# Kernel optimization log

Hardware: AMD Instinct MI355X
Metric: run time of the kernel (lower is better)

Reference implementation:

```python
import jax, jax.numpy as jnp
import numpy as np
import math

B, N, CS, CZ, CH, H, PQK, PV = 1, 1024, 384, 128, 16, 12, 4, 8
INF, EPS = 1e5, 1e-8


def quat_to_rot(q):
    w, x, y, z = q[..., 0], q[..., 1], q[..., 2], q[..., 3]
    r = jnp.stack([
        1 - 2 * (y * y + z * z), 2 * (x * y - w * z), 2 * (x * z + w * y),
        2 * (x * y + w * z), 1 - 2 * (x * x + z * z), 2 * (y * z - w * x),
        2 * (x * z - w * y), 2 * (y * z + w * x), 1 - 2 * (x * x + y * y),
    ], axis=-1)
    return r.reshape(q.shape[:-1] + (3, 3))


def setup_inputs() -> dict:
    key = jax.random.key(0)
    ks = jax.random.split(key, 12)
    sc = 0.02
    s = jax.random.normal(ks[0], (B, N, CS), jnp.float32)
    z = jax.random.normal(ks[1], (B, N, N, CZ), jnp.float32)
    quat = jax.random.normal(ks[2], (B, N, 4), jnp.float32)
    rot = quat_to_rot(quat / jnp.linalg.norm(quat, axis=-1, keepdims=True))
    trans = jax.random.normal(ks[3], (B, N, 3), jnp.float32)
    mask = jnp.ones((B, N), jnp.float32)
    wq = jax.random.normal(ks[4], (CS, H * CH), jnp.float32) * sc
    bq = jnp.zeros((H * CH,), jnp.float32)
    wkv = jax.random.normal(ks[5], (CS, 2 * H * CH), jnp.float32) * sc
    bkv = jnp.zeros((2 * H * CH,), jnp.float32)
    wqp = jax.random.normal(ks[6], (CS, H * PQK * 3), jnp.float32) * sc
    bqp = jnp.zeros((H * PQK * 3,), jnp.float32)
    wkvp = jax.random.normal(ks[7], (CS, H * (PQK + PV) * 3), jnp.float32) * sc
    bkvp = jnp.zeros((H * (PQK + PV) * 3,), jnp.float32)
    wb = jax.random.normal(ks[8], (CZ, H), jnp.float32) * sc
    bb = jnp.zeros((H,), jnp.float32)
    head_w = jax.random.normal(ks[9], (H,), jnp.float32) * 0.1 + 0.5413  # softplus^-1(1)
    dcat = H * (CZ + CH + PV * 4)
    wout = jax.random.normal(ks[10], (dcat, CS), jnp.float32) * sc
    bout = jnp.zeros((CS,), jnp.float32)
    return dict(s=s, z=z, rot=rot, trans=trans, mask=mask, wq=wq, bq=bq,
                wkv=wkv, bkv=bkv, wqp=wqp, bqp=bqp, wkvp=wkvp, bkvp=bkvp,
                wb=wb, bb=bb, head_w=head_w, wout=wout, bout=bout)


def reference(s, z, rot, trans, mask, wq, bq, wkv, bkv, wqp, bqp, wkvp, bkvp,
              wb, bb, head_w, wout, bout):
    # scalar q/k/v: [B,N,H,CH]
    q = (s @ wq + bq).reshape(B, N, H, CH)
    kv = (s @ wkv + bkv).reshape(B, N, H, 2 * CH)
    k, v = kv[..., :CH], kv[..., CH:]

    def make_pts(raw, P):
        # raw layout: [x-coords | y-coords | z-coords], each of width H*P
        pts = jnp.swapaxes(raw.reshape(B, N, 3, H * P), -1, -2)  # [B,N,H*P,3]
        pts = jnp.einsum('bnxy,bnpy->bnpx', rot, pts) + trans[:, :, None, :]
        return pts.reshape(B, N, H, P, 3)

    q_pts = make_pts(s @ wqp + bqp, PQK)                 # [B,N,H,PQK,3] global frame
    kv_pts = make_pts(s @ wkvp + bkvp, PQK + PV)
    k_pts, v_pts = kv_pts[..., :PQK, :], kv_pts[..., PQK:, :]

    # scalar attention + pair bias: [B,H,N,N]
    a = jnp.einsum('bihc,bjhc->bhij', q, k) * math.sqrt(1.0 / (3 * CH))
    bias = z @ wb + bb                                    # [B,N,N,H]
    a = a + math.sqrt(1.0 / 3) * jnp.transpose(bias, (0, 3, 1, 2))

    # point attention via ||q-k||^2 = |q|^2 + |k|^2 - 2 q.k (summed over pts & xyz)
    hw = jax.nn.softplus(head_w) * math.sqrt(1.0 / (3 * (PQK * 9.0 / 2)))  # [H]
    qn = jnp.sum(q_pts ** 2, axis=(-1, -2))               # [B,N,H]
    kn = jnp.sum(k_pts ** 2, axis=(-1, -2))
    cross = jnp.einsum('bihpx,bjhpx->bhij', q_pts, k_pts)
    sqd = (jnp.transpose(qn, (0, 2, 1))[..., None]
           + jnp.transpose(kn, (0, 2, 1))[:, :, None, :]
           - 2.0 * cross)                                 # [B,H,N,N]
    a = a - 0.5 * hw[None, :, None, None] * sqd

    sqm = INF * (mask[:, :, None] * mask[:, None, :] - 1.0)  # [B,N,N]
    a = jax.nn.softmax(a + sqm[:, None], axis=-1)

    # outputs
    o = jnp.einsum('bhij,bjhc->bihc', a, v).reshape(B, N, H * CH)
    o_pt = jnp.einsum('bhij,bjhpx->bihpx', a, v_pts)      # [B,N,H,PV,3] global
    o_pt = jnp.einsum('bnyx,bnhpy->bnhpx', rot, o_pt - trans[:, :, None, None, :])  # invert_apply
    o_pt_norm = jnp.sqrt(jnp.sum(o_pt ** 2, axis=-1) + EPS).reshape(B, N, H * PV)
    o_pt3 = o_pt.reshape(B, N, H * PV, 3)
    o_pair = jnp.einsum('bhij,bijc->bihc', a, z).reshape(B, N, H * CZ)

    cat = jnp.concatenate(
        [o, o_pt3[..., 0], o_pt3[..., 1], o_pt3[..., 2], o_pt_norm, o_pair], axis=-1)
    return cat @ wout + bout
```

## Files before the change

kernel.cpp:

```cpp
#include <hip/hip_runtime.h>
#include <hip/hip_bf16.h>
#include <math.h>

#define NN   1024
#define CS   384
#define CZ   128
#define HH   12
#define HCH  192
#define QPR  144
#define DCAT 2112
#define PROJW 1152
#define INF_ 100000.0f

#define SC_QK 0.14433756729740643f
#define SC_B  0.5773502691896258f
#define SC_PT 0.13608276348795434f

__device__ __forceinline__ float dot4(float4 a, float4 b) {
  return a.x * b.x + a.y * b.y + a.z * b.z + a.w * b.w;
}
__device__ __forceinline__ float bf2f(unsigned short u) {
  unsigned int v = ((unsigned int)u) << 16;
  float f; __builtin_memcpy(&f, &v, 4); return f;
}
__device__ __forceinline__ unsigned short f2bf(float f) {
  __hip_bfloat16 h = __float2bfloat16(f);
  unsigned short u; __builtin_memcpy(&u, &h, 2); return u;
}

__global__ void prep(const float* __restrict__ wb, const float* __restrict__ head_w,
                     float* __restrict__ wb_t, float* __restrict__ hw)
{
  int t = threadIdx.x;
  for (int idx = t; idx < CZ * HH; idx += 256) {
    int c = idx % HH == idx % HH ? idx / HH : 0;
    int h = idx - c * HH;
    wb_t[h * CZ + c] = wb[idx];
  }
  if (t < HH) {
    float x = head_w[t];
    float sp = (x > 20.f) ? x : log1pf(__expf(x));
    hw[t] = sp * SC_PT;
  }
}

__global__ __launch_bounds__(256) void proj_all(
    const float* __restrict__ s,
    const float* __restrict__ wq, const float* __restrict__ bq,
    const float* __restrict__ wkv, const float* __restrict__ bkv,
    const float* __restrict__ wqp, const float* __restrict__ bqp,
    const float* __restrict__ wkvp, const float* __restrict__ bkvp,
    float* __restrict__ proj)
{
  __shared__ float s_lds[8 * CS];
  const int n0 = blockIdx.x * 8;
  for (int idx = threadIdx.x; idx < 8 * CS; idx += 256)
    s_lds[idx] = s[(size_t)(n0 + idx / CS) * CS + (idx % CS)];
  __syncthreads();

  const int gc = blockIdx.y * 128 + (threadIdx.x & 31) * 4;
  const int rg = threadIdx.x >> 5;
  const float* wp; const float* bp; int OUT, lc;
  if (gc < 192)      { wp = wq;   bp = bq;   OUT = 192; lc = gc; }
  else if (gc < 576) { wp = wkv;  bp = bkv;  OUT = 384; lc = gc - 192; }
  else if (gc < 720) { wp = wqp;  bp = bqp;  OUT = 144; lc = gc - 576; }
  else               { wp = wkvp; bp = bkvp; OUT = 432; lc = gc - 720; }

  float a0 = 0.f, a1 = 0.f, a2 = 0.f, a3 = 0.f;
  const float* srow = &s_lds[rg * CS];
#pragma unroll 4
  for (int kk = 0; kk < CS; kk++) {
    float sv = srow[kk];
    float4 w4 = *reinterpret_cast<const float4*>(&wp[(size_t)kk * OUT + lc]);
    a0 += sv * w4.x; a1 += sv * w4.y; a2 += sv * w4.z; a3 += sv * w4.w;
  }
  float* o = proj + (size_t)(n0 + rg) * PROJW + gc;
  o[0] = a0 + bp[lc]; o[1] = a1 + bp[lc + 1];
  o[2] = a2 + bp[lc + 2]; o[3] = a3 + bp[lc + 3];
}

__global__ __launch_bounds__(256) void ipa_transform(
    const float* __restrict__ proj, const float* __restrict__ rot,
    const float* __restrict__ trans,
    float* __restrict__ kc, float* __restrict__ vc,
    float* __restrict__ q_pts, float* __restrict__ kpc,
    float* __restrict__ vpc, float* __restrict__ qn, float* __restrict__ knc)
{
  const int n = blockIdx.x, tid = threadIdx.x;
  const float* pr = proj + (size_t)n * PROJW;
  __shared__ float R[9], T[3], sq_q[48], sq_k[48];
  if (tid < 9) R[tid] = rot[n * 9 + tid];
  if (tid < 3) T[tid] = trans[n * 3 + tid];
  __syncthreads();
  if (tid < HCH) {
    int h = tid >> 4, c = tid & 15;
    kc[(size_t)(h * 16 + c) * NN + n] = pr[192 + h * 32 + c];
    vc[(size_t)(h * 16 + c) * NN + n] = pr[192 + h * 32 + 16 + c];
  }
  if (tid < 48) {
    float r0 = pr[576 + tid], r1 = pr[576 + 48 + tid], r2 = pr[576 + 96 + tid];
    float x = R[0] * r0 + R[1] * r1 + R[2] * r2 + T[0];
    float y = R[3] * r0 + R[4] * r1 + R[5] * r2 + T[1];
    float z = R[6] * r0 + R[7] * r1 + R[8] * r2 + T[2];
    q_pts[(size_t)n * QPR + tid * 3 + 0] = x;
    q_pts[(size_t)n * QPR + tid * 3 + 1] = y;
    q_pts[(size_t)n * QPR + tid * 3 + 2] = z;
    sq_q[tid] = x * x + y * y + z * z;
  }
  if (tid >= 64 && tid < 208) {
    int t = tid - 64;
    float r0 = pr[720 + t], r1 = pr[720 + 144 + t], r2 = pr[720 + 288 + t];
    float x = R[0] * r0 + R[1] * r1 + R[2] * r2 + T[0];
    float y = R[3] * r0 + R[4] * r1 + R[5] * r2 + T[1];
    float z = R[6] * r0 + R[7] * r1 + R[8] * r2 + T[2];
    int h = t / 12, pp = t % 12;
    if (pp < 4) {
      int d = pp * 3;
      kpc[(size_t)(h * 12 + d + 0) * NN + n] = x;
      kpc[(size_t)(h * 12 + d + 1) * NN + n] = y;
      kpc[(size_t)(h * 12 + d + 2) * NN + n] = z;
      sq_k[h * 4 + pp] = x * x + y * y + z * z;
    } else {
      int d = (pp - 4) * 3;
      vpc[(size_t)(h * 24 + d + 0) * NN + n] = x;
      vpc[(size_t)(h * 24 + d + 1) * NN + n] = y;
      vpc[(size_t)(h * 24 + d + 2) * NN + n] = z;
    }
  }
  __syncthreads();
  if (tid < HH) {
    float a = 0.f, b = 0.f;
#pragma unroll
    for (int p = 0; p < 4; p++) { a += sq_q[tid * 4 + p]; b += sq_k[tid * 4 + p]; }
    qn[n * HH + tid] = a;
    knc[(size_t)tid * NN + n] = b;
  }
}

__global__ __launch_bounds__(256) void bias_pass(
    const float* __restrict__ z, const float* __restrict__ wb_t,
    __hip_bfloat16* __restrict__ B)
{
  __shared__ float wb_s[HH * CZ];
  __shared__ float bias_s[HH * 128];
  const int i = blockIdx.y;
  const int jb = blockIdx.x * 128;
  const int tid = threadIdx.x;
  const int jl = tid >> 2, csub = tid & 3;

  for (int e = tid; e < HH * CZ; e += 256) wb_s[e] = wb_t[e];
  __syncthreads();

  const float* zb = z + ((size_t)i * NN + jb + jl) * CZ + csub * 4;
  float4 zq0[8], zq1[8];
#pragma unroll
  for (int k8 = 0; k8 < 8; k8++)
    zq0[k8] = *reinterpret_cast<const float4*>(&zb[k8 * 16]);
#pragma unroll
  for (int k8 = 0; k8 < 8; k8++)
    zq1[k8] = *reinterpret_cast<const float4*>(&zb[(size_t)64 * CZ + k8 * 16]);

  float bd0[HH], bd1[HH];
#pragma unroll
  for (int h = 0; h < HH; h++) { bd0[h] = 0.f; bd1[h] = 0.f; }

#pragma unroll
  for (int k8 = 0; k8 < 8; k8++) {
    const int c = csub * 4 + k8 * 16;
#pragma unroll
    for (int h = 0; h < HH; h++) {
      float4 wv = *reinterpret_cast<const float4*>(&wb_s[h * CZ + c]);
      bd0[h] += dot4(zq0[k8], wv);
      bd1[h] += dot4(zq1[k8], wv);
    }
  }
#pragma unroll
  for (int h = 0; h < HH; h++) {
    bd0[h] += __shfl_xor(bd0[h], 1); bd0[h] += __shfl_xor(bd0[h], 2);
    bd1[h] += __shfl_xor(bd1[h], 1); bd1[h] += __shfl_xor(bd1[h], 2);
  }
  if (csub == 0) {
#pragma unroll
    for (int h = 0; h < HH; h++) {
      bias_s[h * 128 + jl] = bd0[h];
      bias_s[h * 128 + 64 + jl] = bd1[h];
    }
  }
  __syncthreads();
  for (int e = tid; e < HH * 128; e += 256) {
    int h = e >> 7, j2 = e & 127;
    B[((size_t)i * HH + h) * NN + jb + j2] = __float2bfloat16(bias_s[e]);
  }
}

__global__ __launch_bounds__(256) void ipa_attn(
    const float* __restrict__ kc, const float* __restrict__ kpc,
    const float* __restrict__ knc, const float* __restrict__ vc,
    const float* __restrict__ vpc, const float* __restrict__ proj,
    const float* __restrict__ q_pts, const float* __restrict__ qn,
    const float* __restrict__ bb, const float* __restrict__ hw,
    const float* __restrict__ mask,
    __hip_bfloat16* __restrict__ A, float* __restrict__ cat,
    float* __restrict__ optb)
{
  const int h = blockIdx.y;
  const int i = blockIdx.x * 4 + (threadIdx.x >> 6);
  const int lane = threadIdx.x & 63;

  const float* qb = proj + (size_t)i * PROJW + h * 16;
  const float4 q0 = *reinterpret_cast<const float4*>(qb);
  const float4 q1 = *reinterpret_cast<const float4*>(qb + 4);
  const float4 q2 = *reinterpret_cast<const float4*>(qb + 8);
  const float4 q3 = *reinterpret_cast<const float4*>(qb + 12);
  const float* pb = q_pts + (size_t)i * QPR + h * 12;
  const float4 p0 = *reinterpret_cast<const float4*>(pb);
  const float4 p1 = *reinterpret_cast<const float4*>(pb + 4);
  const float4 p2 = *reinterpret_cast<const float4*>(pb + 8);
  const float qnv = qn[i * HH + h];
  const float bbv = bb[h];
  const float hwv = hw[h];
  const float mi = mask[i];

  const float* kch  = kc  + (size_t)h * 16 * NN;
  const float* kpch = kpc + (size_t)h * 12 * NN;
  const float* knch = knc + (size_t)h * NN;
  const float* vch  = vc  + (size_t)h * 16 * NN;
  const float* vpch = vpc + (size_t)h * 24 * NN;
  __hip_bfloat16* Arow = A + ((size_t)i * HH + h) * NN;

  float4 av[4];
#pragma unroll
  for (int t = 0; t < 4; t++) {
    const int j = t * 256 + lane * 4;
    float4 d = {0, 0, 0, 0};
#pragma unroll
    for (int c = 0; c < 16; c++) {
      const float qc = (c < 4 ? (&q0.x)[c] : c < 8 ? (&q1.x)[c - 4]
                       : c < 12 ? (&q2.x)[c - 8] : (&q3.x)[c - 12]);
      float4 kv = *reinterpret_cast<const float4*>(&kch[(size_t)c * NN + j]);
      d.x += qc * kv.x; d.y += qc * kv.y; d.z += qc * kv.z; d.w += qc * kv.w;
    }
    float4 cr = {0, 0, 0, 0};
#pragma unroll
    for (int dd = 0; dd < 12; dd++) {
      const float pc = (dd < 4 ? (&p0.x)[dd] : dd < 8 ? (&p1.x)[dd - 4]
                        : (&p2.x)[dd - 8]);
      float4 kv = *reinterpret_cast<const float4*>(&kpch[(size_t)dd * NN + j]);
      cr.x += pc * kv.x; cr.y += pc * kv.y; cr.z += pc * kv.z; cr.w += pc * kv.w;
    }
    float4 kn4 = *reinterpret_cast<const float4*>(&knch[j]);
    ushort4 bu = *reinterpret_cast<const ushort4*>(&Arow[j]);
    float4 m4 = *reinterpret_cast<const float4*>(&mask[j]);
    av[t].x = SC_QK * d.x + SC_B * (bf2f(bu.x) + bbv)
              - 0.5f * hwv * (qnv + kn4.x - 2.f * cr.x) + INF_ * (mi * m4.x - 1.f);
    av[t].y = SC_QK * d.y + SC_B * (bf2f(bu.y) + bbv)
              - 0.5f * hwv * (qnv + kn4.y - 2.f * cr.y) + INF_ * (mi * m4.y - 1.f);
    av[t].z = SC_QK * d.z + SC_B * (bf2f(bu.z) + bbv)
              - 0.5f * hwv * (qnv + kn4.z - 2.f * cr.z) + INF_ * (mi * m4.z - 1.f);
    av[t].w = SC_QK * d.w + SC_B * (bf2f(bu.w) + bbv)
              - 0.5f * hwv * (qnv + kn4.w - 2.f * cr.w) + INF_ * (mi * m4.w - 1.f);
  }

  float m = av[0].x;
#pragma unroll
  for (int t = 0; t < 4; t++) {
    m = fmaxf(m, av[t].x); m = fmaxf(m, av[t].y);
    m = fmaxf(m, av[t].z); m = fmaxf(m, av[t].w);
  }
  for (int off = 32; off; off >>= 1) m = fmaxf(m, __shfl_xor(m, off));
  float ssum = 0.f;
#pragma unroll
  for (int t = 0; t < 4; t++) {
    av[t].x = __expf(av[t].x - m); ssum += av[t].x;
    av[t].y = __expf(av[t].y - m); ssum += av[t].y;
    av[t].z = __expf(av[t].z - m); ssum += av[t].z;
    av[t].w = __expf(av[t].w - m); ssum += av[t].w;
  }
  for (int off = 32; off; off >>= 1) ssum += __shfl_xor(ssum, off);
  const float inv = 1.f / ssum;
#pragma unroll
  for (int t = 0; t < 4; t++) {
    const int j = t * 256 + lane * 4;
    av[t].x *= inv; av[t].y *= inv; av[t].z *= inv; av[t].w *= inv;
    ushort4 st;
    st.x = f2bf(av[t].x); st.y = f2bf(av[t].y);
    st.z = f2bf(av[t].z); st.w = f2bf(av[t].w);
    *reinterpret_cast<ushort4*>(&Arow[j]) = st;
  }

  float oacc[16], wacc[24];
#pragma unroll
  for (int c = 0; c < 16; c++) oacc[c] = 0.f;
#pragma unroll
  for (int d = 0; d < 24; d++) wacc[d] = 0.f;
#pragma unroll
  for (int t = 0; t < 4; t++) {
    const int j = t * 256 + lane * 4;
    const float4 a4 = av[t];
#pragma unroll
    for (int c = 0; c < 16; c++) {
      float4 vv = *reinterpret_cast<const float4*>(&vch[(size_t)c * NN + j]);
      oacc[c] += dot4(a4, vv);
    }
#pragma unroll
    for (int d = 0; d < 24; d++) {
      float4 wv = *reinterpret_cast<const float4*>(&vpch[(size_t)d * NN + j]);
      wacc[d] += dot4(a4, wv);
    }
  }
  for (int off = 32; off; off >>= 1) {
#pragma unroll
    for (int c = 0; c < 16; c++) oacc[c] += __shfl_xor(oacc[c], off);
#pragma unroll
    for (int d = 0; d < 24; d++) wacc[d] += __shfl_xor(wacc[d], off);
  }
  if (lane == 0) {
    float* cr = cat + (size_t)i * DCAT + h * 16;
#pragma unroll
    for (int c = 0; c < 16; c++) cr[c] = oacc[c];
    float* ob = optb + ((size_t)i * HH + h) * 24;
#pragma unroll
    for (int d = 0; d < 24; d++) ob[d] = wacc[d];
  }
}

__global__ __launch_bounds__(256) void opair_pass(
    const float* __restrict__ z, const __hip_bfloat16* __restrict__ A,
    float* __restrict__ partial)
{
  __shared__ float A_ls[256 * HH];
  __shared__ float red[HH * CZ];
  const int sp = blockIdx.x, i = blockIdx.y;
  const int jb = sp * 256;
  const int tid = threadIdx.x;
  const int c4 = (tid & 31) * 4, jsub = tid >> 5;

  for (int e = tid; e < HH * 64; e += 256) {
    int h = e >> 6, j4 = (e & 63) * 4;
    ushort4 au = *reinterpret_cast<const ushort4*>(
        &A[((size_t)i * HH + h) * NN + jb + j4]);
    A_ls[(j4 + 0) * HH + h] = bf2f(au.x);
    A_ls[(j4 + 1) * HH + h] = bf2f(au.y);
    A_ls[(j4 + 2) * HH + h] = bf2f(au.z);
    A_ls[(j4 + 3) * HH + h] = bf2f(au.w);
  }
  for (int e = tid; e < HH * CZ; e += 256) red[e] = 0.f;
  __syncthreads();

  float4 acc[HH];
#pragma unroll
  for (int h = 0; h < HH; h++) acc[h] = make_float4(0.f, 0.f, 0.f, 0.f);

  const float* zrow = z + ((size_t)i * NN + jb + jsub * 32) * CZ + c4;
  const float* arow = &A_ls[jsub * 32 * HH];
  for (int j0 = 0; j0 < 32; j0 += 4) {
#pragma unroll
    for (int jj = 0; jj < 4; jj++) {
      const int j = j0 + jj;
      float4 zq = *reinterpret_cast<const float4*>(&zrow[(size_t)j * CZ]);
      float4 a0 = *reinterpret_cast<const float4*>(&arow[j * HH]);
      float4 a1 = *reinterpret_cast<const float4*>(&arow[j * HH + 4]);
      float4 a2 = *reinterpret_cast<const float4*>(&arow[j * HH + 8]);
      acc[0].x += a0.x * zq.x; acc[0].y += a0.x * zq.y;
      acc[0].z += a0.x * zq.z; acc[0].w += a0.x * zq.w;
      acc[1].x += a0.y * zq.x; acc[1].y += a0.y * zq.y;
      acc[1].z += a0.y * zq.z; acc[1].w += a0.y * zq.w;
      acc[2].x += a0.z * zq.x; acc[2].y += a0.z * zq.y;
      acc[2].z += a0.z * zq.z; acc[2].w += a0.z * zq.w;
      acc[3].x += a0.w * zq.x; acc[3].y += a0.w * zq.y;
      acc[3].z += a0.w * zq.z; acc[3].w += a0.w * zq.w;
      acc[4].x += a1.x * zq.x; acc[4].y += a1.x * zq.y;
      acc[4].z += a1.x * zq.z; acc[4].w += a1.x * zq.w;
      acc[5].x += a1.y * zq.x; acc[5].y += a1.y * zq.y;
      acc[5].z += a1.y * zq.z; acc[5].w += a1.y * zq.w;
      acc[6].x += a1.z * zq.x; acc[6].y += a1.z * zq.y;
      acc[6].z += a1.z * zq.z; acc[6].w += a1.z * zq.w;
      acc[7].x += a1.w * zq.x; acc[7].y += a1.w * zq.y;
      acc[7].z += a1.w * zq.z; acc[7].w += a1.w * zq.w;
      acc[8].x += a2.x * zq.x; acc[8].y += a2.x * zq.y;
      acc[8].z += a2.x * zq.z; acc[8].w += a2.x * zq.w;
      acc[9].x += a2.y * zq.x; acc[9].y += a2.y * zq.y;
      acc[9].z += a2.y * zq.z; acc[9].w += a2.y * zq.w;
      acc[10].x += a2.z * zq.x; acc[10].y += a2.z * zq.y;
      acc[10].z += a2.z * zq.z; acc[10].w += a2.z * zq.w;
      acc[11].x += a2.w * zq.x; acc[11].y += a2.w * zq.y;
      acc[11].z += a2.w * zq.z; acc[11].w += a2.w * zq.w;
    }
  }
  for (int s = 0; s < 8; s++) {
    __syncthreads();
    if (jsub == s) {
#pragma unroll
      for (int h = 0; h < HH; h++) {
        red[h * CZ + c4 + 0] += acc[h].x;
        red[h * CZ + c4 + 1] += acc[h].y;
        red[h * CZ + c4 + 2] += acc[h].z;
        red[h * CZ + c4 + 3] += acc[h].w;
      }
    }
  }
  __syncthreads();
  float* pp = partial + ((size_t)(i * 4 + sp)) * (HH * CZ);
  for (int e = tid; e < HH * CZ; e += 256) pp[e] = red[e];
}

__global__ __launch_bounds__(256) void opair_reduce(
    const float* __restrict__ partial, const float* __restrict__ optb,
    const float* __restrict__ rot, const float* __restrict__ trans,
    float* __restrict__ cat)
{
  const int i = blockIdx.x, tid = threadIdx.x;
  __shared__ float R_s[9], T_s[3];
  if (tid < 9) R_s[tid] = rot[i * 9 + tid];
  if (tid < 3) T_s[tid] = trans[i * 3 + tid];
  __syncthreads();

  const float* pp = partial + ((size_t)i * 4) * (HH * CZ);
  for (int e = tid; e < HH * CZ; e += 256) {
    float v = pp[e] + pp[HH * CZ + e] + pp[2 * HH * CZ + e] + pp[3 * HH * CZ + e];
    cat[(size_t)i * DCAT + 576 + e] = v;
  }
  if (tid < 96) {
    int h = tid >> 3, p = tid & 7;
    const float* ob = optb + ((size_t)i * HH + h) * 24 + p * 3;
    float gx = ob[0] - T_s[0];
    float gy = ob[1] - T_s[1];
    float gz = ob[2] - T_s[2];
    float lx = R_s[0] * gx + R_s[3] * gy + R_s[6] * gz;
    float ly = R_s[1] * gx + R_s[4] * gy + R_s[7] * gz;
    float lz = R_s[2] * gx + R_s[5] * gy + R_s[8] * gz;
    float* catr = cat + (size_t)i * DCAT;
    catr[192 + 0 * 96 + h * 8 + p] = lx;
    catr[192 + 1 * 96 + h * 8 + p] = ly;
    catr[192 + 2 * 96 + h * 8 + p] = lz;
    catr[480 + h * 8 + p] = sqrtf(lx * lx + ly * ly + lz * lz + 1e-8f);
  }
}

__global__ __launch_bounds__(256) void out_gemm(
    const float* __restrict__ cat, const float* __restrict__ wout,
    const float* __restrict__ bout, float* __restrict__ out)
{
  __shared__ float c_lds[4 * DCAT];
  const int n0 = blockIdx.x * 4;
  const int cq = blockIdx.y * 128 + (threadIdx.x & 63) * 2;
  const int rg = threadIdx.x >> 6;
  for (int idx = threadIdx.x; idx < 4 * DCAT; idx += 256) {
    int r = idx / DCAT, kk = idx - r * DCAT;
    c_lds[idx] = cat[(size_t)(n0 + r) * DCAT + kk];
  }
  __syncthreads();
  float a0 = 0.f, a1 = 0.f;
  const float* crow = &c_lds[rg * DCAT];
#pragma unroll 4
  for (int kk = 0; kk < DCAT; kk++) {
    float cv = crow[kk];
    float2 w2 = *reinterpret_cast<const float2*>(&wout[(size_t)kk * CS + cq]);
    a0 += cv * w2.x; a1 += cv * w2.y;
  }
  float* o = out + (size_t)(n0 + rg) * CS + cq;
  o[0] = a0 + bout[cq]; o[1] = a1 + bout[cq + 1];
}

extern "C" void kernel_launch(void* const* d_in, const int* in_sizes, int n_in,
                              void* d_out, int out_size, void* d_ws, size_t ws_size,
                              hipStream_t stream) {
  const float* s      = (const float*)d_in[0];
  const float* z      = (const float*)d_in[1];
  const float* rot    = (const float*)d_in[2];
  const float* trans  = (const float*)d_in[3];
  const float* mask   = (const float*)d_in[4];
  const float* wq     = (const float*)d_in[5];
  const float* bq     = (const float*)d_in[6];
  const float* wkv    = (const float*)d_in[7];
  const float* bkv    = (const float*)d_in[8];
  const float* wqp    = (const float*)d_in[9];
  const float* bqp    = (const float*)d_in[10];
  const float* wkvp   = (const float*)d_in[11];
  const float* bkvp   = (const float*)d_in[12];
  const float* wb     = (const float*)d_in[13];
  const float* bb     = (const float*)d_in[14];
  const float* head_w = (const float*)d_in[15];
  const float* wout   = (const float*)d_in[16];
  const float* bout   = (const float*)d_in[17];
  float* out = (float*)d_out;

  float* ws = (float*)d_ws;
  float* proj_buf = ws;
  float* kc_buf   = proj_buf + (size_t)NN * PROJW;
  float* vc_buf   = kc_buf + (size_t)HH * 16 * NN;
  float* kpc_buf  = vc_buf + (size_t)HH * 16 * NN;
  float* vpc_buf  = kpc_buf + (size_t)HH * 12 * NN;
  float* knc_buf  = vpc_buf + (size_t)HH * 24 * NN;
  float* qpts_buf = knc_buf + (size_t)HH * NN;
  float* qn_buf   = qpts_buf + (size_t)NN * QPR;
  float* wbt_buf  = qn_buf + NN * HH;
  float* hw_buf   = wbt_buf + HH * CZ;
  float* optb_buf = hw_buf + 16;
  float* cat_buf  = optb_buf + (size_t)NN * HH * 24;
  float* part_buf = cat_buf + (size_t)NN * DCAT;
  __hip_bfloat16* A_buf =
      (__hip_bfloat16*)(part_buf + (size_t)4 * NN * HH * CZ);

  prep<<<dim3(1), dim3(256), 0, stream>>>(wb, head_w, wbt_buf, hw_buf);
  proj_all<<<dim3(NN / 8, 9), dim3(256), 0, stream>>>(
      s, wq, bq, wkv, bkv, wqp, bqp, wkvp, bkvp, proj_buf);
  ipa_transform<<<dim3(NN), dim3(256), 0, stream>>>(
      proj_buf, rot, trans, kc_buf, vc_buf, qpts_buf, kpc_buf, vpc_buf,
      qn_buf, knc_buf);
  bias_pass<<<dim3(8, NN), dim3(256), 0, stream>>>(z, wbt_buf, A_buf);
  ipa_attn<<<dim3(NN / 4, HH), dim3(256), 0, stream>>>(
      kc_buf, kpc_buf, knc_buf, vc_buf, vpc_buf, proj_buf, qpts_buf,
      qn_buf, bb, hw_buf, mask, A_buf, cat_buf, optb_buf);
  opair_pass<<<dim3(4, NN), dim3(256), 0, stream>>>(z, A_buf, part_buf);
  opair_reduce<<<dim3(NN), dim3(256), 0, stream>>>(
      part_buf, optb_buf, rot, trans, cat_buf);
  out_gemm<<<dim3(NN / 4, 3), dim3(256), 0, stream>>>(
      cat_buf, wout, bout, out);
}
```

Measured before the change: 731.0 us.

## Store K/V caches in bf16, drop prep kernel, reverse opair row order

The key, value and point caches read by ipa_attn are now stored as bf16 instead of fp32, which halves the bytes those loops fetch. The prep kernel is removed: bias_pass transposes wb itself, and ipa_attn computes the softplus head weight inline, saving one launch. opair_pass now walks rows in reverse, likely so that z rows still cached from bias_pass are reused. The bf16 caches lower the accuracy of the logits and outputs.

```diff
diff --git a/kernel.cpp b/kernel.cpp
--- a/kernel.cpp
+++ b/kernel.cpp
@@ -27,21 +27,8 @@
   __hip_bfloat16 h = __float2bfloat16(f);
   unsigned short u; __builtin_memcpy(&u, &h, 2); return u;
 }
-
-__global__ void prep(const float* __restrict__ wb, const float* __restrict__ head_w,
-                     float* __restrict__ wb_t, float* __restrict__ hw)
-{
-  int t = threadIdx.x;
-  for (int idx = t; idx < CZ * HH; idx += 256) {
-    int c = idx % HH == idx % HH ? idx / HH : 0;
-    int h = idx - c * HH;
-    wb_t[h * CZ + c] = wb[idx];
-  }
-  if (t < HH) {
-    float x = head_w[t];
-    float sp = (x > 20.f) ? x : log1pf(__expf(x));
-    hw[t] = sp * SC_PT;
-  }
+__device__ __forceinline__ float4 bf4(ushort4 u) {
+  return make_float4(bf2f(u.x), bf2f(u.y), bf2f(u.z), bf2f(u.w));
 }
 
 __global__ __launch_bounds__(256) void proj_all(
@@ -82,9 +69,10 @@
 __global__ __launch_bounds__(256) void ipa_transform(
     const float* __restrict__ proj, const float* __restrict__ rot,
     const float* __restrict__ trans,
-    float* __restrict__ kc, float* __restrict__ vc,
-    float* __restrict__ q_pts, float* __restrict__ kpc,
-    float* __restrict__ vpc, float* __restrict__ qn, float* __restrict__ knc)
+    unsigned short* __restrict__ kc, unsigned short* __restrict__ vc,
+    float* __restrict__ q_pts, unsigned short* __restrict__ kpc,
+    unsigned short* __restrict__ vpc, float* __restrict__ qn,
+    float* __restrict__ knc)
 {
   const int n = blockIdx.x, tid = threadIdx.x;
   const float* pr = proj + (size_t)n * PROJW;
@@ -94,8 +82,8 @@
   __syncthreads();
   if (tid < HCH) {
     int h = tid >> 4, c = tid & 15;
-    kc[(size_t)(h * 16 + c) * NN + n] = pr[192 + h * 32 + c];
-    vc[(size_t)(h * 16 + c) * NN + n] = pr[192 + h * 32 + 16 + c];
+    kc[(size_t)(h * 16 + c) * NN + n] = f2bf(pr[192 + h * 32 + c]);
+    vc[(size_t)(h * 16 + c) * NN + n] = f2bf(pr[192 + h * 32 + 16 + c]);
   }
   if (tid < 48) {
     float r0 = pr[576 + tid], r1 = pr[576 + 48 + tid], r2 = pr[576 + 96 + tid];
@@ -116,15 +104,15 @@
     int h = t / 12, pp = t % 12;
     if (pp < 4) {
       int d = pp * 3;
-      kpc[(size_t)(h * 12 + d + 0) * NN + n] = x;
-      kpc[(size_t)(h * 12 + d + 1) * NN + n] = y;
-      kpc[(size_t)(h * 12 + d + 2) * NN + n] = z;
+      kpc[(size_t)(h * 12 + d + 0) * NN + n] = f2bf(x);
+      kpc[(size_t)(h * 12 + d + 1) * NN + n] = f2bf(y);
+      kpc[(size_t)(h * 12 + d + 2) * NN + n] = f2bf(z);
       sq_k[h * 4 + pp] = x * x + y * y + z * z;
     } else {
       int d = (pp - 4) * 3;
-      vpc[(size_t)(h * 24 + d + 0) * NN + n] = x;
-      vpc[(size_t)(h * 24 + d + 1) * NN + n] = y;
-      vpc[(size_t)(h * 24 + d + 2) * NN + n] = z;
+      vpc[(size_t)(h * 24 + d + 0) * NN + n] = f2bf(x);
+      vpc[(size_t)(h * 24 + d + 1) * NN + n] = f2bf(y);
+      vpc[(size_t)(h * 24 + d + 2) * NN + n] = f2bf(z);
     }
   }
   __syncthreads();
@@ -138,7 +126,7 @@
 }
 
 __global__ __launch_bounds__(256) void bias_pass(
-    const float* __restrict__ z, const float* __restrict__ wb_t,
+    const float* __restrict__ z, const float* __restrict__ wb,
     __hip_bfloat16* __restrict__ B)
 {
   __shared__ float wb_s[HH * CZ];
@@ -148,7 +136,10 @@
   const int tid = threadIdx.x;
   const int jl = tid >> 2, csub = tid & 3;
 
-  for (int e = tid; e < HH * CZ; e += 256) wb_s[e] = wb_t[e];
+  for (int e = tid; e < HH * CZ; e += 256) {
+    int c = e / HH, h = e - c * HH;
+    wb_s[h * CZ + c] = wb[e];
+  }
   __syncthreads();
 
   const float* zb = z + ((size_t)i * NN + jb + jl) * CZ + csub * 4;
@@ -194,11 +185,11 @@
 }
 
 __global__ __launch_bounds__(256) void ipa_attn(
-    const float* __restrict__ kc, const float* __restrict__ kpc,
-    const float* __restrict__ knc, const float* __restrict__ vc,
-    const float* __restrict__ vpc, const float* __restrict__ proj,
+    const unsigned short* __restrict__ kc, const unsigned short* __restrict__ kpc,
+    const float* __restrict__ knc, const unsigned short* __restrict__ vc,
+    const unsigned short* __restrict__ vpc, const float* __restrict__ proj,
     const float* __restrict__ q_pts, const float* __restrict__ qn,
-    const float* __restrict__ bb, const float* __restrict__ hw,
+    const float* __restrict__ bb, const float* __restrict__ head_w,
     const float* __restrict__ mask,
     __hip_bfloat16* __restrict__ A, float* __restrict__ cat,
     float* __restrict__ optb)
@@ -218,14 +209,15 @@
   const float4 p2 = *reinterpret_cast<const float4*>(pb + 8);
   const float qnv = qn[i * HH + h];
   const float bbv = bb[h];
-  const float hwv = hw[h];
+  const float xw = head_w[h];
+  const float hwv = ((xw > 20.f) ? xw : log1pf(__expf(xw))) * SC_PT;
   const float mi = mask[i];
 
-  const float* kch  = kc  + (size_t)h * 16 * NN;
-  const float* kpch = kpc + (size_t)h * 12 * NN;
-  const float* knch = knc + (size_t)h * NN;
-  const float* vch  = vc  + (size_t)h * 16 * NN;
-  const float* vpch = vpc + (size_t)h * 24 * NN;
+  const unsigned short* kch  = kc  + (size_t)h * 16 * NN;
+  const unsigned short* kpch = kpc + (size_t)h * 12 * NN;
+  const float*          knch = knc + (size_t)h * NN;
+  const unsigned short* vch  = vc  + (size_t)h * 16 * NN;
+  const unsigned short* vpch = vpc + (size_t)h * 24 * NN;
   __hip_bfloat16* Arow = A + ((size_t)i * HH + h) * NN;
 
   float4 av[4];
@@ -237,7 +229,7 @@
     for (int c = 0; c < 16; c++) {
       const float qc = (c < 4 ? (&q0.x)[c] : c < 8 ? (&q1.x)[c - 4]
                        : c < 12 ? (&q2.x)[c - 8] : (&q3.x)[c - 12]);
-      float4 kv = *reinterpret_cast<const float4*>(&kch[(size_t)c * NN + j]);
+      float4 kv = bf4(*reinterpret_cast<const ushort4*>(&kch[(size_t)c * NN + j]));
       d.x += qc * kv.x; d.y += qc * kv.y; d.z += qc * kv.z; d.w += qc * kv.w;
     }
     float4 cr = {0, 0, 0, 0};
@@ -245,7 +237,7 @@
     for (int dd = 0; dd < 12; dd++) {
       const float pc = (dd < 4 ? (&p0.x)[dd] : dd < 8 ? (&p1.x)[dd - 4]
                         : (&p2.x)[dd - 8]);
-      float4 kv = *reinterpret_cast<const float4*>(&kpch[(size_t)dd * NN + j]);
+      float4 kv = bf4(*reinterpret_cast<const ushort4*>(&kpch[(size_t)dd * NN + j]));
       cr.x += pc * kv.x; cr.y += pc * kv.y; cr.z += pc * kv.z; cr.w += pc * kv.w;
     }
     float4 kn4 = *reinterpret_cast<const float4*>(&knch[j]);
@@ -299,12 +291,12 @@
     const float4 a4 = av[t];
 #pragma unroll
     for (int c = 0; c < 16; c++) {
-      float4 vv = *reinterpret_cast<const float4*>(&vch[(size_t)c * NN + j]);
+      float4 vv = bf4(*reinterpret_cast<const ushort4*>(&vch[(size_t)c * NN + j]));
       oacc[c] += dot4(a4, vv);
     }
 #pragma unroll
     for (int d = 0; d < 24; d++) {
-      float4 wv = *reinterpret_cast<const float4*>(&vpch[(size_t)d * NN + j]);
+      float4 wv = bf4(*reinterpret_cast<const ushort4*>(&vpch[(size_t)d * NN + j]));
       wacc[d] += dot4(a4, wv);
     }
   }
@@ -330,7 +322,7 @@
 {
   __shared__ float A_ls[256 * HH];
   __shared__ float red[HH * CZ];
-  const int sp = blockIdx.x, i = blockIdx.y;
+  const int sp = blockIdx.x, i = NN - 1 - blockIdx.y;
   const int jb = sp * 256;
   const int tid = threadIdx.x;
   const int c4 = (tid & 31) * 4, jsub = tid >> 5;
@@ -487,31 +479,28 @@
 
   float* ws = (float*)d_ws;
   float* proj_buf = ws;
-  float* kc_buf   = proj_buf + (size_t)NN * PROJW;
-  float* vc_buf   = kc_buf + (size_t)HH * 16 * NN;
-  float* kpc_buf  = vc_buf + (size_t)HH * 16 * NN;
-  float* vpc_buf  = kpc_buf + (size_t)HH * 12 * NN;
-  float* knc_buf  = vpc_buf + (size_t)HH * 24 * NN;
+  unsigned short* kc_buf  = (unsigned short*)(proj_buf + (size_t)NN * PROJW);
+  unsigned short* vc_buf  = (unsigned short*)(proj_buf + (size_t)NN * PROJW + 196608);
+  unsigned short* kpc_buf = (unsigned short*)(proj_buf + (size_t)NN * PROJW + 393216);
+  unsigned short* vpc_buf = (unsigned short*)(proj_buf + (size_t)NN * PROJW + 540672);
+  float* knc_buf  = proj_buf + (size_t)NN * PROJW + 835584;
   float* qpts_buf = knc_buf + (size_t)HH * NN;
   float* qn_buf   = qpts_buf + (size_t)NN * QPR;
-  float* wbt_buf  = qn_buf + NN * HH;
-  float* hw_buf   = wbt_buf + HH * CZ;
-  float* optb_buf = hw_buf + 16;
+  float* optb_buf = qn_buf + NN * HH + 16;
   float* cat_buf  = optb_buf + (size_t)NN * HH * 24;
   float* part_buf = cat_buf + (size_t)NN * DCAT;
   __hip_bfloat16* A_buf =
       (__hip_bfloat16*)(part_buf + (size_t)4 * NN * HH * CZ);
 
-  prep<<<dim3(1), dim3(256), 0, stream>>>(wb, head_w, wbt_buf, hw_buf);
   proj_all<<<dim3(NN / 8, 9), dim3(256), 0, stream>>>(
       s, wq, bq, wkv, bkv, wqp, bqp, wkvp, bkvp, proj_buf);
   ipa_transform<<<dim3(NN), dim3(256), 0, stream>>>(
       proj_buf, rot, trans, kc_buf, vc_buf, qpts_buf, kpc_buf, vpc_buf,
       qn_buf, knc_buf);
-  bias_pass<<<dim3(8, NN), dim3(256), 0, stream>>>(z, wbt_buf, A_buf);
+  bias_pass<<<dim3(8, NN), dim3(256), 0, stream>>>(z, wb, A_buf);
   ipa_attn<<<dim3(NN / 4, HH), dim3(256), 0, stream>>>(
       kc_buf, kpc_buf, knc_buf, vc_buf, vpc_buf, proj_buf, qpts_buf,
-      qn_buf, bb, hw_buf, mask, A_buf, cat_buf, optb_buf);
+      qn_buf, bb, head_w, mask, A_buf, cat_buf, optb_buf);
   opair_pass<<<dim3(4, NN), dim3(256), 0, stream>>>(z, A_buf, part_buf);
   opair_reduce<<<dim3(NN), dim3(256), 0, stream>>>(
       part_buf, optb_buf, rot, trans, cat_buf);
```

Result: slower. 870.1 us (+19.0%).
